# Kernel tuning notes

Hardware: AMD Instinct MI355X
Metric: run time of the kernel (lower is better)

## Reference

```python
import jax, jax.numpy as jnp
import numpy as np

HIDDEN = 768
NUM_BLOCKS = 8
BLOCK = HIDDEN // NUM_BLOCKS
LAMBDA = 0.01
SCALE = 0.02


def softshrink(v, lam):
    return jnp.sign(v) * jnp.maximum(jnp.abs(v) - lam, 0.0)


def setup_inputs() -> dict:
    key = jax.random.key(0)
    ks = jax.random.split(key, 5)
    B, S = 4, 8192
    x = jax.random.normal(ks[0], (B, S, HIDDEN), dtype=jnp.float32)
    w1 = SCALE * jax.random.normal(ks[1], (2, NUM_BLOCKS, BLOCK, BLOCK), dtype=jnp.float32)
    b1 = SCALE * jax.random.normal(ks[2], (2, NUM_BLOCKS, BLOCK), dtype=jnp.float32)
    w2 = SCALE * jax.random.normal(ks[3], (2, NUM_BLOCKS, BLOCK, BLOCK), dtype=jnp.float32)
    b2 = SCALE * jax.random.normal(ks[4], (2, NUM_BLOCKS, BLOCK), dtype=jnp.float32)
    return {"x": x, "w1": w1, "b1": b1, "w2": w2, "b2": b2}


def reference(x, w1, b1, w2, b2):
    bias = x
    dtype = x.dtype
    xf = x.astype(jnp.float32)
    B, S, C = xf.shape
    M = S // 2 + 1  # total modes; hard_thresholding_fraction=1.0 -> all kept
    X = jnp.fft.rfft(xf, axis=1, norm="ortho")  # [B, M, C] complex64
    X = X.reshape(B, M, NUM_BLOCKS, BLOCK)
    xr, xi = X.real, X.imag
    # layer 1: complex block-diagonal matmul + relu
    mul = lambda inp, w: jnp.einsum("bmnd,ndk->bmnk", inp, w)
    o1r = jax.nn.relu(mul(xr, w1[0]) - mul(xi, w1[1]) + b1[0])
    o1i = jax.nn.relu(mul(xi, w1[0]) + mul(xr, w1[1]) + b1[1])
    # layer 2
    o2r = mul(o1r, w2[0]) - mul(o1i, w2[1]) + b2[0]
    o2i = mul(o1r, w2[1]) + mul(o1i, w2[0]) + b2[1]
    # softshrink applied elementwise to real and imag parts
    o2r = softshrink(o2r, LAMBDA)
    o2i = softshrink(o2i, LAMBDA)
    Y = (o2r + 1j * o2i).reshape(B, M, C)
    y = jnp.fft.irfft(Y, n=S, axis=1, norm="ortho").astype(dtype)
    return y + bias
```

## Files before the change

kernel.cpp:

```cpp
#include <hip/hip_runtime.h>
#include <hip/hip_bf16.h>

#define HIDDEN 768
#define NB 8
#define BLK 96
#define S_LEN 8192
#define H_LEN 4096
#define M_LEN 4097
#define MP 4160
#define BATCH 4
#define KBIG 192
#define TMOD 64
#define APITCH 100

#define TWO_PI 6.28318530717958647692f
#define INV_SQRT_N 0.011048543456039806f
#define C_INV 0.022097086912079612f
#define LAM 0.01f

typedef __attribute__((ext_vector_type(8))) short short8;
typedef __attribute__((ext_vector_type(4))) float float4v;

__device__ __forceinline__ short f2bf(float f) {
    __hip_bfloat16 h = __float2bfloat16(f);
    return *reinterpret_cast<short*>(&h);
}
__device__ __forceinline__ float bf2f(unsigned short s) {
    __hip_bfloat16 h = *reinterpret_cast<__hip_bfloat16*>(&s);
    return __bfloat162float(h);
}
__device__ __forceinline__ unsigned pack2bf(float a, float b) {
    return (unsigned)(unsigned short)f2bf(a) | ((unsigned)(unsigned short)f2bf(b) << 16);
}
__device__ __forceinline__ float2 cmul(float2 a, float2 b) {
    return make_float2(a.x * b.x - a.y * b.y, a.x * b.y + a.y * b.x);
}

__global__ __launch_bounds__(256) void prep_weights(const float* __restrict__ w1,
                                                    const float* __restrict__ w2,
                                                    const float* __restrict__ b1,
                                                    const float* __restrict__ b2,
                                                    short* __restrict__ WT1,
                                                    short* __restrict__ WT2,
                                                    float* __restrict__ bb1,
                                                    float* __restrict__ bb2) {
    int idx = blockIdx.x * 256 + threadIdx.x;
    if (idx < NB * KBIG * KBIG) {
        int n = idx / (KBIG * KBIG);
        int r = idx % (KBIG * KBIG);
        int op = r / KBIG;
        int kin = r % KBIG;
        int oc = op >> 1;
        int oim = op & 1;
        int d = kin >> 1;
        int im = kin & 1;
        {
            float w0 = w1[((size_t)(0 * NB + n) * BLK + d) * BLK + oc];
            float wi = w1[((size_t)(1 * NB + n) * BLK + d) * BLK + oc];
            float v = oim ? (im ? w0 : wi) : (im ? -wi : w0);
            WT1[idx] = f2bf(v);
        }
        {
            float w0 = w2[((size_t)(0 * NB + n) * BLK + d) * BLK + oc];
            float wi = w2[((size_t)(1 * NB + n) * BLK + d) * BLK + oc];
            float v = oim ? (im ? w0 : wi) : (im ? -wi : w0);
            WT2[idx] = f2bf(v);
        }
    }
    if (idx < NB * KBIG) {
        int n = idx / KBIG, op = idx % KBIG;
        int oc = op >> 1, oim = op & 1;
        bb1[idx] = oim ? b1[(1 * NB + n) * BLK + oc] : b1[(0 * NB + n) * BLK + oc];
        bb2[idx] = oim ? b2[(1 * NB + n) * BLK + oc] : b2[(0 * NB + n) * BLK + oc];
    }
}

__global__ __launch_bounds__(256) void init_twiddles(float2* __restrict__ tw4k,
                                                     float2* __restrict__ tw8k) {
    int i = blockIdx.x * 256 + threadIdx.x;
    if (i < 4096) {
        float ang = -TWO_PI * (float)i * (1.0f / 4096.0f);
        tw4k[i] = make_float2(cosf(ang), sinf(ang));
    }
    if (i <= 4096) {
        float ang = -TWO_PI * (float)i * (1.0f / 8192.0f);
        tw8k[i] = make_float2(cosf(ang), sinf(ang));
    }
}

__global__ __launch_bounds__(256) void transpose_in(const float* __restrict__ x,
                                                    __hip_bfloat16* __restrict__ xT) {
    __shared__ float t[64][66];
    const int cb = blockIdx.x, sb = blockIdx.y, b = blockIdx.z;
    const int tid = threadIdx.x;
    {
        const int cq = tid & 15, sr = tid >> 4;
        const float* xp = x + ((size_t)(b * S_LEN + sb * 64 + sr)) * HIDDEN + cb * 64 + cq * 4;
        #pragma unroll
        for (int i = 0; i < 4; i++) {
            float4 v = *(const float4*)(xp + (size_t)16 * i * HIDDEN);
            int s = sr + 16 * i;
            t[cq * 4 + 0][s] = v.x;
            t[cq * 4 + 1][s] = v.y;
            t[cq * 4 + 2][s] = v.z;
            t[cq * 4 + 3][s] = v.w;
        }
    }
    __syncthreads();
    {
        const int s4 = tid & 15, cr = tid >> 4;
        #pragma unroll
        for (int i = 0; i < 4; i++) {
            int c = cr + 16 * i;
            float2 a = *(const float2*)&t[c][s4 * 4];
            float2 bv = *(const float2*)&t[c][s4 * 4 + 2];
            short4 o;
            o.x = f2bf(a.x); o.y = f2bf(a.y); o.z = f2bf(bv.x); o.w = f2bf(bv.y);
            *(short4*)(xT + ((size_t)(b * HIDDEN + cb * 64 + c)) * S_LEN + sb * 64 + s4 * 4) = o;
        }
    }
}

template<bool INV>
__device__ __forceinline__ void dft16(float2* v) {
    const float s3 = INV ? -1.f : 1.f;
    constexpr float C1 = 0.92387953251128674f;
    constexpr float S1 = 0.38268343236508977f;
    constexpr float R2 = 0.70710678118654752f;
    float2 a[16];
    #pragma unroll
    for (int na = 0; na < 4; na++) {
        float2 x0 = v[na], x1 = v[na + 4], x2 = v[na + 8], x3 = v[na + 12];
        float t0x = x0.x + x2.x, t0y = x0.y + x2.y;
        float t1x = x0.x - x2.x, t1y = x0.y - x2.y;
        float t2x = x1.x + x3.x, t2y = x1.y + x3.y;
        float t3x = x1.x - x3.x, t3y = x1.y - x3.y;
        a[na]      = make_float2(t0x + t2x, t0y + t2y);
        a[na + 8]  = make_float2(t0x - t2x, t0y - t2y);
        a[na + 4]  = make_float2(t1x + s3 * t3y, t1y - s3 * t3x);
        a[na + 12] = make_float2(t1x - s3 * t3y, t1y + s3 * t3x);
    }
    auto tw = [s3](float2 z, float ce, float se) {
        return make_float2(z.x * ce + s3 * z.y * se, z.y * ce - s3 * z.x * se);
    };
    a[5]  = tw(a[5],  C1,  S1);
    a[6]  = tw(a[6],  R2,  R2);
    a[7]  = tw(a[7],  S1,  C1);
    a[9]  = tw(a[9],  R2,  R2);
    a[10] = tw(a[10], 0.f, 1.f);
    a[11] = tw(a[11], -R2, R2);
    a[13] = tw(a[13], S1,  C1);
    a[14] = tw(a[14], -R2, R2);
    a[15] = tw(a[15], -C1, -S1);
    #pragma unroll
    for (int kb = 0; kb < 4; kb++) {
        float2 x0 = a[4 * kb], x1 = a[4 * kb + 1], x2 = a[4 * kb + 2], x3 = a[4 * kb + 3];
        float t0x = x0.x + x2.x, t0y = x0.y + x2.y;
        float t1x = x0.x - x2.x, t1y = x0.y - x2.y;
        float t2x = x1.x + x3.x, t2y = x1.y + x3.y;
        float t3x = x1.x - x3.x, t3y = x1.y - x3.y;
        v[kb]      = make_float2(t0x + t2x, t0y + t2y);
        v[kb + 8]  = make_float2(t0x - t2x, t0y - t2y);
        v[kb + 4]  = make_float2(t1x + s3 * t3y, t1y - s3 * t3x);
        v[kb + 12] = make_float2(t1x - s3 * t3y, t1y + s3 * t3x);
    }
}

template<bool INV>
__device__ __forceinline__ void fft3pass(float2* v, float2* arr,
                                         const float2* __restrict__ tw4k, int t) {
    const int n0 = t & 15;
    const int hi = t >> 4;

    float2 w1 = tw4k[t];
    if (INV) w1.y = -w1.y;
    dft16<INV>(v);
    arr[n0 * 17 + hi] = v[0];
    {
        float2 wp = w1;
        #pragma unroll
        for (int p = 1; p < 16; p++) {
            arr[(n0 + 16 * p) * 17 + hi] = cmul(v[p], wp);
            wp = cmul(wp, w1);
        }
    }
    __syncthreads();

    #pragma unroll
    for (int n1 = 0; n1 < 16; n1++) v[n1] = arr[t * 17 + n1];
    __syncthreads();
    dft16<INV>(v);
    float2 w2 = tw4k[16 * n0];
    if (INV) w2.y = -w2.y;
    arr[hi * 17 + n0] = v[0];
    {
        float2 wp = w2;
        #pragma unroll
        for (int q = 1; q < 16; q++) {
            arr[(hi + 16 * q) * 17 + n0] = cmul(v[q], wp);
            wp = cmul(wp, w2);
        }
    }
    __syncthreads();

    #pragma unroll
    for (int i = 0; i < 16; i++) v[i] = arr[t * 17 + i];
    dft16<INV>(v);
}

__global__ __launch_bounds__(256, 4) void fft_fwd(const __hip_bfloat16* __restrict__ xT,
                                                  unsigned int* __restrict__ Xc,
                                                  const float2* __restrict__ tw4k,
                                                  const float2* __restrict__ tw8k) {
    __shared__ __align__(16) float2 arr[256 * 17];
    const int wg = blockIdx.x;
    const int t = threadIdx.x;
    const __hip_bfloat162* xrow = (const __hip_bfloat162*)(xT + (size_t)wg * S_LEN);

    float2 v[16];
    #pragma unroll
    for (int j = 0; j < 16; j++) {
        __hip_bfloat162 pz = xrow[t + 256 * j];
        v[j] = make_float2(__bfloat162float(pz.x), __bfloat162float(pz.y));
    }

    fft3pass<false>(v, arr, tw4k, t);

    __syncthreads();
    #pragma unroll
    for (int k0 = 0; k0 < 16; k0++) arr[t + 256 * k0] = v[k0];
    __syncthreads();

    unsigned int* Xrow = Xc + (size_t)wg * MP;
    for (int m = t; m <= H_LEN; m += 256) {
        int ia = m & (H_LEN - 1);
        int ib = (H_LEN - m) & (H_LEN - 1);
        float2 za = arr[ia];
        float2 zb = arr[ib];
        float er = 0.5f * (za.x + zb.x), ei = 0.5f * (za.y - zb.y);
        float dr = za.x - zb.x, di = za.y + zb.y;
        float or_ = 0.5f * di, oi = -0.5f * dr;
        float2 tt = tw8k[m];
        float xrv = (er + tt.x * or_ - tt.y * oi) * INV_SQRT_N;
        float xiv = (ei + tt.x * oi + tt.y * or_) * INV_SQRT_N;
        unsigned wd = (unsigned short)f2bf(xrv) | ((unsigned)(unsigned short)f2bf(xiv) << 16);
        Xrow[m] = wd;
    }
}

__global__ __launch_bounds__(256, 3) void mlp_mfma(const short* __restrict__ WT1,
                                                   const short* __restrict__ WT2,
                                                   const float* __restrict__ bb1,
                                                   const float* __restrict__ bb2,
                                                   unsigned int* __restrict__ Xc) {
    __shared__ __align__(16) unsigned int actA[TMOD * APITCH];
    __shared__ __align__(16) unsigned int actB[TMOD * APITCH];
    const int tid = threadIdx.x;
    const int chunk = blockIdx.x;
    const int n = blockIdx.y;
    const int b = blockIdx.z;
    const int m0 = chunk * TMOD;
    unsigned int* __restrict__ Xrow0 =
        Xc + ((size_t)b * HIDDEN + (size_t)n * BLK) * MP + m0;

    const int w = tid >> 6;
    const int l15 = tid & 15;
    const int q = (tid >> 4) & 3;
    const int outw = w * 48;
    const int mstg = tid & 63;

    #pragma unroll
    for (int dp = 0; dp < 6; dp++) {
        int d0 = dp * 16 + w * 4;
        uint4 vv;
        vv.x = Xrow0[(size_t)(d0 + 0) * MP + mstg];
        vv.y = Xrow0[(size_t)(d0 + 1) * MP + mstg];
        vv.z = Xrow0[(size_t)(d0 + 2) * MP + mstg];
        vv.w = Xrow0[(size_t)(d0 + 3) * MP + mstg];
        *(uint4*)&actA[mstg * APITCH + d0] = vv;
    }

    short8 wf[3][6];
    for (int nl = 0; nl < 3; nl++)
        for (int ks = 0; ks < 6; ks++)
            wf[nl][ks] = *(const short8*)(WT1 + ((size_t)n * KBIG + outw + nl * 16 + l15) * KBIG + ks * 32 + q * 8);

    __syncthreads();

    for (int mt = 0; mt < 4; mt++) {
        float4v acc[3];
        for (int nl = 0; nl < 3; nl++)
            acc[nl] = *(const float4v*)(bb1 + n * KBIG + outw + nl * 16 + q * 4);
        #pragma unroll
        for (int ks = 0; ks < 6; ks++) {
            short8 bf = *(const short8*)(&actA[(mt * 16 + l15) * APITCH + ks * 16 + q * 4]);
            acc[0] = __builtin_amdgcn_mfma_f32_16x16x32_bf16(wf[0][ks], bf, acc[0], 0, 0, 0);
            acc[1] = __builtin_amdgcn_mfma_f32_16x16x32_bf16(wf[1][ks], bf, acc[1], 0, 0, 0);
            acc[2] = __builtin_amdgcn_mfma_f32_16x16x32_bf16(wf[2][ks], bf, acc[2], 0, 0, 0);
        }
        #pragma unroll
        for (int nl = 0; nl < 3; nl++) {
            uint2 st;
            st.x = pack2bf(fmaxf(acc[nl][0], 0.f), fmaxf(acc[nl][1], 0.f));
            st.y = pack2bf(fmaxf(acc[nl][2], 0.f), fmaxf(acc[nl][3], 0.f));
            *(uint2*)&actB[(mt * 16 + l15) * APITCH + outw / 2 + nl * 8 + q * 2] = st;
        }
    }

    short8 wf2[3][6];
    for (int nl = 0; nl < 3; nl++)
        for (int ks = 0; ks < 6; ks++)
            wf2[nl][ks] = *(const short8*)(WT2 + ((size_t)n * KBIG + outw + nl * 16 + l15) * KBIG + ks * 32 + q * 8);

    __syncthreads();

    for (int mt = 0; mt < 4; mt++) {
        float4v acc[3];
        for (int nl = 0; nl < 3; nl++)
            acc[nl] = *(const float4v*)(bb2 + n * KBIG + outw + nl * 16 + q * 4);
        #pragma unroll
        for (int ks = 0; ks < 6; ks++) {
            short8 bf = *(const short8*)(&actB[(mt * 16 + l15) * APITCH + ks * 16 + q * 4]);
            acc[0] = __builtin_amdgcn_mfma_f32_16x16x32_bf16(wf2[0][ks], bf, acc[0], 0, 0, 0);
            acc[1] = __builtin_amdgcn_mfma_f32_16x16x32_bf16(wf2[1][ks], bf, acc[1], 0, 0, 0);
            acc[2] = __builtin_amdgcn_mfma_f32_16x16x32_bf16(wf2[2][ks], bf, acc[2], 0, 0, 0);
        }
        #pragma unroll
        for (int nl = 0; nl < 3; nl++) {
            float v0 = acc[nl][0], v1 = acc[nl][1], v2 = acc[nl][2], v3 = acc[nl][3];
            v0 = copysignf(fmaxf(fabsf(v0) - LAM, 0.f), v0);
            v1 = copysignf(fmaxf(fabsf(v1) - LAM, 0.f), v1);
            v2 = copysignf(fmaxf(fabsf(v2) - LAM, 0.f), v2);
            v3 = copysignf(fmaxf(fabsf(v3) - LAM, 0.f), v3);
            uint2 st;
            st.x = pack2bf(v0, v1);
            st.y = pack2bf(v2, v3);
            *(uint2*)&actA[(mt * 16 + l15) * APITCH + outw / 2 + nl * 8 + q * 2] = st;
        }
    }
    __syncthreads();

    #pragma unroll
    for (int dp = 0; dp < 6; dp++) {
        int d0 = dp * 16 + w * 4;
        uint4 vv = *(const uint4*)&actA[mstg * APITCH + d0];
        Xrow0[(size_t)(d0 + 0) * MP + mstg] = vv.x;
        Xrow0[(size_t)(d0 + 1) * MP + mstg] = vv.y;
        Xrow0[(size_t)(d0 + 2) * MP + mstg] = vv.z;
        Xrow0[(size_t)(d0 + 3) * MP + mstg] = vv.w;
    }
}

__global__ __launch_bounds__(256, 4) void fft_inv(const unsigned int* __restrict__ Xc,
                                                  __hip_bfloat16* __restrict__ yT,
                                                  const float2* __restrict__ tw4k,
                                                  const float2* __restrict__ tw8k) {
    __shared__ __align__(16) float2 arr[256 * 17];
    const int wg = blockIdx.x;
    const int t = threadIdx.x;
    const unsigned int* Xrow = Xc + (size_t)wg * MP;

    float2 v[16];
    #pragma unroll
    for (int j = 0; j < 16; j++) {
        int m = t + 256 * j;
        unsigned va = Xrow[m];
        unsigned vb = Xrow[H_LEN - m];
        float arv = bf2f((unsigned short)(va & 0xFFFF));
        float aiv = bf2f((unsigned short)(va >> 16));
        float brv = bf2f((unsigned short)(vb & 0xFFFF));
        float biv = bf2f((unsigned short)(vb >> 16));
        if (m == 0) { aiv = 0.f; biv = 0.f; }
        float er = 0.5f * (arv + brv), ei = 0.5f * (aiv - biv);
        float dr = arv - brv, di = aiv + biv;
        float2 tt = tw8k[m];
        float wcs = tt.x, wsn = -tt.y;
        float or_ = 0.5f * (wcs * dr - wsn * di);
        float oi = 0.5f * (wcs * di + wsn * dr);
        v[j] = make_float2(er - oi, ei + or_);
    }

    fft3pass<true>(v, arr, tw4k, t);

    __hip_bfloat162* orow = (__hip_bfloat162*)(yT + (size_t)wg * S_LEN);
    #pragma unroll
    for (int k0 = 0; k0 < 16; k0++) {
        __hip_bfloat162 w;
        w.x = __float2bfloat16(C_INV * v[k0].x);
        w.y = __float2bfloat16(C_INV * v[k0].y);
        orow[t + 256 * k0] = w;
    }
}

__global__ __launch_bounds__(256) void add_out(const __hip_bfloat16* __restrict__ yT,
                                               const float* __restrict__ x,
                                               float* __restrict__ out) {
    __shared__ float t[64][66];
    const int cb = blockIdx.x, sb = blockIdx.y, b = blockIdx.z;
    const int tid = threadIdx.x;
    {
        const int s4 = tid & 15, cr = tid >> 4;
        #pragma unroll
        for (int i = 0; i < 4; i++) {
            int c = cr + 16 * i;
            short4 v = *(const short4*)(yT + ((size_t)(b * HIDDEN + cb * 64 + c)) * S_LEN + sb * 64 + s4 * 4);
            t[s4 * 4 + 0][c] = bf2f((unsigned short)v.x);
            t[s4 * 4 + 1][c] = bf2f((unsigned short)v.y);
            t[s4 * 4 + 2][c] = bf2f((unsigned short)v.z);
            t[s4 * 4 + 3][c] = bf2f((unsigned short)v.w);
        }
    }
    __syncthreads();
    {
        const int cq = tid & 15, sr = tid >> 4;
        #pragma unroll
        for (int i = 0; i < 4; i++) {
            int s = sr + 16 * i;
            const size_t off = ((size_t)(b * S_LEN + sb * 64 + s)) * HIDDEN + cb * 64 + cq * 4;
            float4 xv = *(const float4*)(x + off);
            float2 a = *(const float2*)&t[s][cq * 4];
            float2 bv = *(const float2*)&t[s][cq * 4 + 2];
            float4 ov;
            ov.x = xv.x + a.x; ov.y = xv.y + a.y; ov.z = xv.z + bv.x; ov.w = xv.w + bv.y;
            *(float4*)(out + off) = ov;
        }
    }
}

extern "C" void kernel_launch(void* const* d_in, const int* in_sizes, int n_in,
                              void* d_out, int out_size, void* d_ws, size_t ws_size,
                              hipStream_t stream) {
    const float* x  = (const float*)d_in[0];
    const float* w1 = (const float*)d_in[1];
    const float* b1 = (const float*)d_in[2];
    const float* w2 = (const float*)d_in[3];
    const float* b2 = (const float*)d_in[4];
    float* out = (float*)d_out;

    char* p = (char*)d_ws;
    __hip_bfloat16* xT = (__hip_bfloat16*)p;           p += (size_t)BATCH * HIDDEN * S_LEN * 2;
    unsigned int*   Xc = (unsigned int*)p;             p += (size_t)BATCH * HIDDEN * MP * 4;
    short* WT1 = (short*)p;                            p += (size_t)NB * KBIG * KBIG * 2;
    short* WT2 = (short*)p;                            p += (size_t)NB * KBIG * KBIG * 2;
    float* bb1 = (float*)p;                            p += (size_t)NB * KBIG * 4;
    float* bb2 = (float*)p;                            p += (size_t)NB * KBIG * 4;
    float2* tw4k = (float2*)p;                         p += (size_t)4096 * sizeof(float2);
    float2* tw8k = (float2*)p;                         p += (size_t)4100 * sizeof(float2);

    prep_weights<<<(NB * KBIG * KBIG + 255) / 256, 256, 0, stream>>>(
        w1, w2, b1, b2, WT1, WT2, bb1, bb2);

    init_twiddles<<<17, 256, 0, stream>>>(tw4k, tw8k);

    transpose_in<<<dim3(HIDDEN / 64, S_LEN / 64, BATCH), 256, 0, stream>>>(x, xT);

    fft_fwd<<<BATCH * HIDDEN, 256, 0, stream>>>(xT, Xc, tw4k, tw8k);

    mlp_mfma<<<dim3(65, NB, BATCH), 256, 0, stream>>>(WT1, WT2, bb1, bb2, Xc);

    fft_inv<<<BATCH * HIDDEN, 256, 0, stream>>>(Xc, xT , tw4k, tw8k);

    add_out<<<dim3(HIDDEN / 64, S_LEN / 64, BATCH), 256, 0, stream>>>(xT, x, out);
}
```

Before: 350.2 us.

## Process two mode chunks per MLP workgroup, reusing register-held weights

Each MLP workgroup now handles two 64-mode chunks instead of one. Both layers' weight fragments are loaded into registers once up front and reused for both chunks. The grid shrinks from 65 to 33 blocks in x, and the second chunk's staging load is issued before the first chunk's writeback. Holding both weight sets at once raises register pressure, so launch bounds drop to 2 waves per SIMD, which lowers occupancy, and the grid has fewer workgroups.

```diff
diff --git a/kernel.cpp b/kernel.cpp
--- a/kernel.cpp
+++ b/kernel.cpp
@@ -248,7 +248,73 @@
     }
 }
 
-__global__ __launch_bounds__(256, 3) void mlp_mfma(const short* __restrict__ WT1,
+__device__ __forceinline__ void mlp_stage(const unsigned int* __restrict__ Xrow0,
+                                          unsigned int* __restrict__ dst,
+                                          int w, int mstg) {
+    #pragma unroll
+    for (int dp = 0; dp < 6; dp++) {
+        int d0 = dp * 16 + w * 4;
+        uint4 vv;
+        vv.x = Xrow0[(size_t)(d0 + 0) * MP + mstg];
+        vv.y = Xrow0[(size_t)(d0 + 1) * MP + mstg];
+        vv.z = Xrow0[(size_t)(d0 + 2) * MP + mstg];
+        vv.w = Xrow0[(size_t)(d0 + 3) * MP + mstg];
+        *(uint4*)&dst[mstg * APITCH + d0] = vv;
+    }
+}
+
+__device__ __forceinline__ void mlp_writeback(const unsigned int* __restrict__ src,
+                                              unsigned int* __restrict__ Xrow0,
+                                              int w, int mstg) {
+    #pragma unroll
+    for (int dp = 0; dp < 6; dp++) {
+        int d0 = dp * 16 + w * 4;
+        uint4 vv = *(const uint4*)&src[mstg * APITCH + d0];
+        Xrow0[(size_t)(d0 + 0) * MP + mstg] = vv.x;
+        Xrow0[(size_t)(d0 + 1) * MP + mstg] = vv.y;
+        Xrow0[(size_t)(d0 + 2) * MP + mstg] = vv.z;
+        Xrow0[(size_t)(d0 + 3) * MP + mstg] = vv.w;
+    }
+}
+
+template<bool RELU>
+__device__ __forceinline__ void mlp_layer(const unsigned int* __restrict__ src,
+                                          unsigned int* __restrict__ dst,
+                                          const short8 (&wf)[3][6],
+                                          const float* __restrict__ bias,
+                                          int l15, int q, int outw) {
+    for (int mt = 0; mt < 4; mt++) {
+        float4v acc[3];
+        for (int nl = 0; nl < 3; nl++)
+            acc[nl] = *(const float4v*)(bias + outw + nl * 16 + q * 4);
+        #pragma unroll
+        for (int ks = 0; ks < 6; ks++) {
+            short8 bf = *(const short8*)(&src[(mt * 16 + l15) * APITCH + ks * 16 + q * 4]);
+            acc[0] = __builtin_amdgcn_mfma_f32_16x16x32_bf16(wf[0][ks], bf, acc[0], 0, 0, 0);
+            acc[1] = __builtin_amdgcn_mfma_f32_16x16x32_bf16(wf[1][ks], bf, acc[1], 0, 0, 0);
+            acc[2] = __builtin_amdgcn_mfma_f32_16x16x32_bf16(wf[2][ks], bf, acc[2], 0, 0, 0);
+        }
+        #pragma unroll
+        for (int nl = 0; nl < 3; nl++) {
+            float v0 = acc[nl][0], v1 = acc[nl][1], v2 = acc[nl][2], v3 = acc[nl][3];
+            if (RELU) {
+                v0 = fmaxf(v0, 0.f); v1 = fmaxf(v1, 0.f);
+                v2 = fmaxf(v2, 0.f); v3 = fmaxf(v3, 0.f);
+            } else {
+                v0 = copysignf(fmaxf(fabsf(v0) - LAM, 0.f), v0);
+                v1 = copysignf(fmaxf(fabsf(v1) - LAM, 0.f), v1);
+                v2 = copysignf(fmaxf(fabsf(v2) - LAM, 0.f), v2);
+                v3 = copysignf(fmaxf(fabsf(v3) - LAM, 0.f), v3);
+            }
+            uint2 st;
+            st.x = pack2bf(v0, v1);
+            st.y = pack2bf(v2, v3);
+            *(uint2*)&dst[(mt * 16 + l15) * APITCH + outw / 2 + nl * 8 + q * 2] = st;
+        }
+    }
+}
+
+__global__ __launch_bounds__(256, 2) void mlp_mfma(const short* __restrict__ WT1,
                                                    const short* __restrict__ WT2,
                                                    const float* __restrict__ bb1,
                                                    const float* __restrict__ bb2,
@@ -256,12 +322,16 @@
     __shared__ __align__(16) unsigned int actA[TMOD * APITCH];
     __shared__ __align__(16) unsigned int actB[TMOD * APITCH];
     const int tid = threadIdx.x;
-    const int chunk = blockIdx.x;
+    const int cx = blockIdx.x;
     const int n = blockIdx.y;
     const int b = blockIdx.z;
-    const int m0 = chunk * TMOD;
-    unsigned int* __restrict__ Xrow0 =
-        Xc + ((size_t)b * HIDDEN + (size_t)n * BLK) * MP + m0;
+    const int chunkA = 2 * cx;
+    const int chunkB = 2 * cx + 1;
+    const bool hasB = (chunkB < 65);
+    unsigned int* __restrict__ Xbase =
+        Xc + ((size_t)b * HIDDEN + (size_t)n * BLK) * MP;
+    unsigned int* __restrict__ XrowA = Xbase + chunkA * TMOD;
+    unsigned int* __restrict__ XrowB = Xbase + chunkB * TMOD;
 
     const int w = tid >> 6;
     const int l15 = tid & 15;
@@ -269,85 +339,31 @@
     const int outw = w * 48;
     const int mstg = tid & 63;
 
-    #pragma unroll
-    for (int dp = 0; dp < 6; dp++) {
-        int d0 = dp * 16 + w * 4;
-        uint4 vv;
-        vv.x = Xrow0[(size_t)(d0 + 0) * MP + mstg];
-        vv.y = Xrow0[(size_t)(d0 + 1) * MP + mstg];
-        vv.z = Xrow0[(size_t)(d0 + 2) * MP + mstg];
-        vv.w = Xrow0[(size_t)(d0 + 3) * MP + mstg];
-        *(uint4*)&actA[mstg * APITCH + d0] = vv;
-    }
-
-    short8 wf[3][6];
+    mlp_stage(XrowA, actA, w, mstg);
+
+    short8 wf1[3][6], wf2[3][6];
     for (int nl = 0; nl < 3; nl++)
-        for (int ks = 0; ks < 6; ks++)
-            wf[nl][ks] = *(const short8*)(WT1 + ((size_t)n * KBIG + outw + nl * 16 + l15) * KBIG + ks * 32 + q * 8);
-
-    __syncthreads();
-
-    for (int mt = 0; mt < 4; mt++) {
-        float4v acc[3];
-        for (int nl = 0; nl < 3; nl++)
-            acc[nl] = *(const float4v*)(bb1 + n * KBIG + outw + nl * 16 + q * 4);
-        #pragma unroll
         for (int ks = 0; ks < 6; ks++) {
-            short8 bf = *(const short8*)(&actA[(mt * 16 + l15) * APITCH + ks * 16 + q * 4]);
-            acc[0] = __builtin_amdgcn_mfma_f32_16x16x32_bf16(wf[0][ks], bf, acc[0], 0, 0, 0);
-            acc[1] = __builtin_amdgcn_mfma_f32_16x16x32_bf16(wf[1][ks], bf, acc[1], 0, 0, 0);
-            acc[2] = __builtin_amdgcn_mfma_f32_16x16x32_bf16(wf[2][ks], bf, acc[2], 0, 0, 0);
-        }
-        #pragma unroll
-        for (int nl = 0; nl < 3; nl++) {
-            uint2 st;
-            st.x = pack2bf(fmaxf(acc[nl][0], 0.f), fmaxf(acc[nl][1], 0.f));
-            st.y = pack2bf(fmaxf(acc[nl][2], 0.f), fmaxf(acc[nl][3], 0.f));
-            *(uint2*)&actB[(mt * 16 + l15) * APITCH + outw / 2 + nl * 8 + q * 2] = st;
-        }
-    }
-
-    short8 wf2[3][6];
-    for (int nl = 0; nl < 3; nl++)
-        for (int ks = 0; ks < 6; ks++)
+            wf1[nl][ks] = *(const short8*)(WT1 + ((size_t)n * KBIG + outw + nl * 16 + l15) * KBIG + ks * 32 + q * 8);
             wf2[nl][ks] = *(const short8*)(WT2 + ((size_t)n * KBIG + outw + nl * 16 + l15) * KBIG + ks * 32 + q * 8);
-
-    __syncthreads();
-
-    for (int mt = 0; mt < 4; mt++) {
-        float4v acc[3];
-        for (int nl = 0; nl < 3; nl++)
-            acc[nl] = *(const float4v*)(bb2 + n * KBIG + outw + nl * 16 + q * 4);
-        #pragma unroll
-        for (int ks = 0; ks < 6; ks++) {
-            short8 bf = *(const short8*)(&actB[(mt * 16 + l15) * APITCH + ks * 16 + q * 4]);
-            acc[0] = __builtin_amdgcn_mfma_f32_16x16x32_bf16(wf2[0][ks], bf, acc[0], 0, 0, 0);
-            acc[1] = __builtin_amdgcn_mfma_f32_16x16x32_bf16(wf2[1][ks], bf, acc[1], 0, 0, 0);
-            acc[2] = __builtin_amdgcn_mfma_f32_16x16x32_bf16(wf2[2][ks], bf, acc[2], 0, 0, 0);
-        }
-        #pragma unroll
-        for (int nl = 0; nl < 3; nl++) {
-            float v0 = acc[nl][0], v1 = acc[nl][1], v2 = acc[nl][2], v3 = acc[nl][3];
-            v0 = copysignf(fmaxf(fabsf(v0) - LAM, 0.f), v0);
-            v1 = copysignf(fmaxf(fabsf(v1) - LAM, 0.f), v1);
-            v2 = copysignf(fmaxf(fabsf(v2) - LAM, 0.f), v2);
-            v3 = copysignf(fmaxf(fabsf(v3) - LAM, 0.f), v3);
-            uint2 st;
-            st.x = pack2bf(v0, v1);
-            st.y = pack2bf(v2, v3);
-            *(uint2*)&actA[(mt * 16 + l15) * APITCH + outw / 2 + nl * 8 + q * 2] = st;
-        }
-    }
-    __syncthreads();
-
-    #pragma unroll
-    for (int dp = 0; dp < 6; dp++) {
-        int d0 = dp * 16 + w * 4;
-        uint4 vv = *(const uint4*)&actA[mstg * APITCH + d0];
-        Xrow0[(size_t)(d0 + 0) * MP + mstg] = vv.x;
-        Xrow0[(size_t)(d0 + 1) * MP + mstg] = vv.y;
-        Xrow0[(size_t)(d0 + 2) * MP + mstg] = vv.z;
-        Xrow0[(size_t)(d0 + 3) * MP + mstg] = vv.w;
+        }
+
+    __syncthreads();
+    mlp_layer<true >(actA, actB, wf1, bb1 + n * KBIG, l15, q, outw);
+    __syncthreads();
+    mlp_layer<false>(actB, actA, wf2, bb2 + n * KBIG, l15, q, outw);
+    __syncthreads();
+
+    if (hasB) mlp_stage(XrowB, actB, w, mstg);
+    mlp_writeback(actA, XrowA, w, mstg);
+
+    if (hasB) {
+        __syncthreads();
+        mlp_layer<true >(actB, actA, wf1, bb1 + n * KBIG, l15, q, outw);
+        __syncthreads();
+        mlp_layer<false>(actA, actB, wf2, bb2 + n * KBIG, l15, q, outw);
+        __syncthreads();
+        mlp_writeback(actB, XrowB, w, mstg);
     }
 }
 
@@ -456,7 +472,7 @@
 
     fft_fwd<<<BATCH * HIDDEN, 256, 0, stream>>>(xT, Xc, tw4k, tw8k);
 
-    mlp_mfma<<<dim3(65, NB, BATCH), 256, 0, stream>>>(WT1, WT2, bb1, bb2, Xc);
+    mlp_mfma<<<dim3(33, NB, BATCH), 256, 0, stream>>>(WT1, WT2, bb1, bb2, Xc);
 
     fft_inv<<<BATCH * HIDDEN, 256, 0, stream>>>(Xc, xT , tw4k, tw8k);
 
```

Measured after the change: 350.9 us. Within noise of the previous version (+0.2%).
